# Optimization experiments

Hardware: AMD Instinct MI355X
Metric: run time of the kernel (lower is better)

Reference implementation:

```python
import jax, jax.numpy as jnp
import numpy as np

E = 8          # n_routed_experts
TOP_K = 2      # num_experts_per_tok
H = 1024       # hidden_size
I = 512        # moe_intermediate_size
SI = 512       # shared expert intermediate (I * n_shared_experts)
B, S = 4, 4096


def setup_inputs() -> dict:
    key = jax.random.key(0)
    ks = jax.random.split(key, 8)
    sc_h = 1.0 / np.sqrt(H)
    sc_i = 1.0 / np.sqrt(I)
    return {
        "hidden_states": jax.random.normal(ks[0], (B, S, H), jnp.float32),
        "gate_w": jax.random.normal(ks[1], (E, H), jnp.float32) * sc_h,  # router logits weight [E,H]
        "Wg": jax.random.normal(ks[2], (E, H, I), jnp.float32) * sc_h,   # per-expert gate_proj
        "Wu": jax.random.normal(ks[3], (E, H, I), jnp.float32) * sc_h,   # per-expert up_proj
        "Wd": jax.random.normal(ks[4], (E, I, H), jnp.float32) * sc_i,   # per-expert down_proj
        "sWg": jax.random.normal(ks[5], (H, SI), jnp.float32) * sc_h,    # shared expert gate_proj
        "sWu": jax.random.normal(ks[6], (H, SI), jnp.float32) * sc_h,
        "sWd": jax.random.normal(ks[7], (SI, H), jnp.float32) * sc_i,
    }


def reference(hidden_states, gate_w, Wg, Wu, Wd, sWg, sWu, sWd):
    b, s, h = hidden_states.shape
    x = hidden_states.reshape(-1, h)                      # [T,H]

    # ---- MoEGate: softmax scoring + greedy top-k + weight normalization ----
    logits = x.astype(jnp.float32) @ gate_w.T             # [T,E]
    scores = jax.nn.softmax(logits, axis=-1)
    topk_w, topk_idx = jax.lax.top_k(scores, TOP_K)       # [T,K]
    topk_w = topk_w / (topk_w.sum(-1, keepdims=True) + 1e-20)  # norm_topk_prob

    # combine weights as a dense [T,E] map (scatter of topk weights)
    cw = (jax.nn.one_hot(topk_idx, E, dtype=topk_w.dtype) * topk_w[..., None]).sum(1)  # [T,E]

    # ---- routed experts: down(gelu(gate(x)) * up(x)), combined by gate weight ----
    g = jnp.einsum("th,ehi->tei", x, Wg)
    u = jnp.einsum("th,ehi->tei", x, Wu)
    inter = jax.nn.gelu(g, approximate=False) * u         # [T,E,I]
    y = jnp.einsum("tei,te,eih->th", inter, cw.astype(x.dtype), Wd)

    # ---- shared expert on the identity path ----
    sh = (jax.nn.gelu(x @ sWg, approximate=False) * (x @ sWu)) @ sWd

    return (y + sh).reshape(b, s, h)
```

## Files before the change

kernel.cpp:

```cpp
#include <hip/hip_runtime.h>
#include <hip/hip_bf16.h>
#include <math.h>


#define T_TOTAL 16384
#define HDIM 1024
#define IDIM 512
#define NE 9
#define CNT_STRIDE 16

typedef __bf16 bf16x8 __attribute__((ext_vector_type(8)));
typedef float f32x4 __attribute__((ext_vector_type(4)));

typedef __attribute__((address_space(1))) void gvoid_t;
typedef __attribute__((address_space(3))) void lvoid_t;

__device__ __forceinline__ void load_lds16(const void* g, void* l) {
  __builtin_amdgcn_global_load_lds((const gvoid_t*)g, (lvoid_t*)l, 16, 0, 0);
}

__device__ __forceinline__ f32x4 mfma_bf16(bf16x8 a, bf16x8 b, f32x4 c) {
  return __builtin_amdgcn_mfma_f32_16x16x32_bf16(a, b, c, 0, 0, 0);
}

__global__ __launch_bounds__(256) void k_gate(const float* __restrict__ x,
                                              const float* __restrict__ gw,
                                              __bf16* __restrict__ xb,
                                              int* __restrict__ tok,
                                              float* __restrict__ wtl,
                                              int* __restrict__ cnt,
                                              int* __restrict__ inv) {
  __shared__ int s_eid[64][2];
  __shared__ float s_wt[64][2];
  __shared__ int s_rank[64][2];
  __shared__ int lcnt[8];
  __shared__ int lbase[8];
  const int wv = threadIdx.x >> 6, lane = threadIdx.x & 63;
  if (threadIdx.x < 8) lcnt[threadIdx.x] = 0;
  __syncthreads();

  for (int i = 0; i < 16; i++) {
    const int tl = wv * 16 + i;
    const int t = blockIdx.x * 64 + tl;
    const float* xr = x + (size_t)t * HDIM + lane * 16;
    float4 xv[4];
#pragma unroll
    for (int j = 0; j < 4; j++) xv[j] = ((const float4*)xr)[j];

    bf16x8 v0, v1;
#pragma unroll
    for (int j = 0; j < 8; j++) v0[j] = (__bf16)((const float*)xv)[j];
#pragma unroll
    for (int j = 0; j < 8; j++) v1[j] = (__bf16)((const float*)xv)[j + 8];
    bf16x8* xbo = (bf16x8*)(xb + (size_t)t * HDIM + lane * 16);
    xbo[0] = v0;
    xbo[1] = v1;

    float acc[8];
#pragma unroll
    for (int e = 0; e < 8; e++) {
      const float4* gp = (const float4*)(gw + e * HDIM + lane * 16);
      float s = 0.f;
#pragma unroll
      for (int j = 0; j < 4; j++) {
        float4 g = gp[j];
        s += xv[j].x * g.x + xv[j].y * g.y + xv[j].z * g.z + xv[j].w * g.w;
      }
      acc[e] = s;
    }
#pragma unroll
    for (int d = 32; d >= 1; d >>= 1) {
#pragma unroll
      for (int e = 0; e < 8; e++) acc[e] += __shfl_xor(acc[e], d, 64);
    }
    if (lane == 0) {
      float mx = acc[0];
#pragma unroll
      for (int e = 1; e < 8; e++) mx = fmaxf(mx, acc[e]);
      float p[8], Z = 0.f;
#pragma unroll
      for (int e = 0; e < 8; e++) {
        p[e] = expf(acc[e] - mx);
        Z += p[e];
      }
#pragma unroll
      for (int e = 0; e < 8; e++) p[e] /= Z;
      int i1 = 0;
#pragma unroll
      for (int e = 1; e < 8; e++)
        if (p[e] > p[i1]) i1 = e;
      int i2 = (i1 == 0) ? 1 : 0;
#pragma unroll
      for (int e = 0; e < 8; e++)
        if (e != i1 && p[e] > p[i2]) i2 = e;
      const float s12 = p[i1] + p[i2] + 1e-20f;
      s_eid[tl][0] = i1;
      s_eid[tl][1] = i2;
      s_wt[tl][0] = p[i1] / s12;
      s_wt[tl][1] = p[i2] / s12;
    }
  }
  __syncthreads();

  if (threadIdx.x < 64) {
    s_rank[threadIdx.x][0] = atomicAdd(&lcnt[s_eid[threadIdx.x][0]], 1);
    s_rank[threadIdx.x][1] = atomicAdd(&lcnt[s_eid[threadIdx.x][1]], 1);
  }
  __syncthreads();
  if (threadIdx.x < 8)
    lbase[threadIdx.x] =
        atomicAdd(&cnt[threadIdx.x * CNT_STRIDE], lcnt[threadIdx.x]);
  __syncthreads();
  if (threadIdx.x < 64) {
    const int t = blockIdx.x * 64 + threadIdx.x;
#pragma unroll
    for (int j = 0; j < 2; j++) {
      const int e = s_eid[threadIdx.x][j];
      const int slot = lbase[e] + s_rank[threadIdx.x][j];
      tok[e * T_TOTAL + slot] = t;
      wtl[e * T_TOTAL + slot] = s_wt[threadIdx.x][j];
      inv[t * 2 + j] = e * T_TOTAL + slot;
    }
  }
}

__global__ void k_scan(const int* __restrict__ cnt, int* __restrict__ base) {
  if (threadIdx.x == 0 && blockIdx.x == 0) {
    int s = 0;
#pragma unroll
    for (int e = 0; e < 8; e++) {
      base[e] = s;
      s += cnt[e * CNT_STRIDE];
    }
  }
}

__global__ __launch_bounds__(256) void k_transpose64(
    const float* __restrict__ w8, const float* __restrict__ w1,
    __bf16* __restrict__ out) {
  __shared__ float tile[64][65];
  const int b = blockIdx.z;
  const float* src = (b < 8) ? (w8 + (size_t)b * IDIM * HDIM) : w1;
  const int c0 = blockIdx.x * 64, r0 = blockIdx.y * 64;
  const int t = threadIdx.x;

#pragma unroll
  for (int j = 0; j < 4; j++) {
    const int rr = (t >> 4) + j * 16;
    const int cc = (t & 15) * 4;
    const float4 v = *(const float4*)(src + (size_t)(r0 + rr) * HDIM + c0 + cc);
    tile[rr][cc] = v.x;
    tile[rr][cc + 1] = v.y;
    tile[rr][cc + 2] = v.z;
    tile[rr][cc + 3] = v.w;
  }
  __syncthreads();

#pragma unroll
  for (int j = 0; j < 2; j++) {
    const int cidx = (t >> 3) + j * 32;
    const int rseg = (t & 7) * 8;
    bf16x8 v;
#pragma unroll
    for (int k = 0; k < 8; k++) v[k] = (__bf16)tile[rseg + k][cidx];
    *(bf16x8*)(out + (size_t)b * HDIM * IDIM + (size_t)(c0 + cidx) * IDIM + r0 +
               rseg) = v;
  }
}

__global__ __launch_bounds__(256) void k_transpose_fuse64(
    const float* __restrict__ w8, const float* __restrict__ w1,
    __bf16* __restrict__ out, int u16off) {
  __shared__ float tile[64][65];
  const int b = blockIdx.z;
  const float* src = (b < 8) ? (w8 + (size_t)b * HDIM * IDIM) : w1;
  const int c0 = blockIdx.x * 64, r0 = blockIdx.y * 64;
  const int t = threadIdx.x;

#pragma unroll
  for (int j = 0; j < 4; j++) {
    const int rr = (t >> 4) + j * 16;
    const int cc = (t & 15) * 4;
    const float4 v = *(const float4*)(src + (size_t)(r0 + rr) * IDIM + c0 + cc);
    tile[rr][cc] = v.x;
    tile[rr][cc + 1] = v.y;
    tile[rr][cc + 2] = v.z;
    tile[rr][cc + 3] = v.w;
  }
  __syncthreads();

#pragma unroll
  for (int j = 0; j < 2; j++) {
    const int cidx = (t >> 3) + j * 32;
    const int rseg = (t & 7) * 8;
    const int ic = c0 + cidx;
    const int f = 2 * (ic & ~15) + (ic & 15) + u16off;
    bf16x8 v;
#pragma unroll
    for (int k = 0; k < 8; k++) v[k] = (__bf16)tile[rseg + k][cidx];
    *(bf16x8*)(out + (size_t)b * 1024 * HDIM + (size_t)f * HDIM + r0 + rseg) = v;
  }
}

__global__ __launch_bounds__(256, 2) void k_gu(
    const __bf16* __restrict__ xb, const __bf16* __restrict__ Wfu,
    const int* __restrict__ tok, const float* __restrict__ wtl,
    const int* __restrict__ cnt, __bf16* __restrict__ inter, int zbase) {
  const int e = blockIdx.z + zbase;
  const bool se = (e == 8);
  const int cnt_e = se ? T_TOTAL : cnt[e * CNT_STRIDE];
  const int m0 = blockIdx.x * 128;
  if (m0 >= cnt_e) return;

  __shared__ __bf16 sA[128][64];
  __shared__ __bf16 sB[128][64];
  const int tid = threadIdx.x, w = tid >> 6, lane = tid & 63;
  const int n0 = blockIdx.y * 128;
  const int quad = lane >> 4, l16 = lane & 15;
  const int wm = (w & 1) * 64, wn = (w >> 1) * 64;

  const int sr = tid >> 3;
  const int scs = ((tid & 7) ^ (sr & 7)) * 8;
  const __bf16* ap[4];
  const __bf16* bp[4];
#pragma unroll
  for (int sh = 0; sh < 4; sh++) {
    int s = m0 + sh * 32 + sr;
    if (s > cnt_e - 1) s = cnt_e - 1;
    const int t = se ? s : tok[e * T_TOTAL + s];
    ap[sh] = xb + (size_t)t * HDIM + scs;
    bp[sh] = Wfu + ((size_t)e * 1024 + n0 + sh * 32 + sr) * HDIM + scs;
  }
  char* const la = (char*)sA + w * 1024;
  char* const lb = (char*)sB + w * 1024;

  f32x4 acc[4][4];
#pragma unroll
  for (int im = 0; im < 4; im++)
#pragma unroll
    for (int in = 0; in < 4; in++) acc[im][in] = {0.f, 0.f, 0.f, 0.f};

  for (int k = 0; k < HDIM; k += 64) {
    __syncthreads();
#pragma unroll
    for (int sh = 0; sh < 4; sh++) {
      load_lds16(ap[sh], la + sh * 4096);
      load_lds16(bp[sh], lb + sh * 4096);
      ap[sh] += 64;
      bp[sh] += 64;
    }
    __syncthreads();
#pragma unroll
    for (int kh = 0; kh < 2; kh++) {
      bf16x8 af[4], bfr[4];
#pragma unroll
      for (int i = 0; i < 4; i++) {
        const int ra = wm + i * 16 + l16;
        af[i] = *(const bf16x8*)((const char*)sA + ra * 128 +
                                 ((kh * 4 + quad) ^ (ra & 7)) * 16);
        const int rb = wn + i * 16 + l16;
        bfr[i] = *(const bf16x8*)((const char*)sB + rb * 128 +
                                  ((kh * 4 + quad) ^ (rb & 7)) * 16);
      }
#pragma unroll
      for (int im = 0; im < 4; im++)
#pragma unroll
        for (int in = 0; in < 4; in++)
          acc[im][in] = mfma_bf16(af[im], bfr[in], acc[im][in]);
    }
  }

#pragma unroll
  for (int im = 0; im < 4; im++) {
#pragma unroll
    for (int r = 0; r < 4; r++) {
      const int slot = m0 + wm + im * 16 + quad * 4 + r;
      if (slot < cnt_e) {
        const float wt = se ? 1.0f : wtl[e * T_TOTAL + slot];
        __bf16* op =
            inter + ((size_t)e * T_TOTAL + slot) * IDIM + ((n0 + wn) >> 1) + l16;
#pragma unroll
        for (int p = 0; p < 2; p++) {
          const float g = acc[im][2 * p][r];
          const float u = acc[im][2 * p + 1][r];
          const float v =
              wt * u * 0.5f * g * (1.0f + erff(g * 0.70710678118654752f));
          op[p * 16] = (__bf16)v;
        }
      }
    }
  }
}

__global__ __launch_bounds__(256, 2) void k_down_rs(
    const __bf16* __restrict__ inter, const __bf16* __restrict__ WdT,
    const int* __restrict__ cnt, const int* __restrict__ base,
    float* __restrict__ yb) {
  const int e = blockIdx.z;
  const int cnt_e = cnt[e * CNT_STRIDE];
  const int m0 = blockIdx.x * 128;
  if (m0 >= cnt_e) return;
  const int rowb = base[e];

  __shared__ __bf16 sA[128][64];
  __shared__ __bf16 sB[128][64];
  const int tid = threadIdx.x, w = tid >> 6, lane = tid & 63;
  const int n0 = blockIdx.y * 128;
  const int quad = lane >> 4, l16 = lane & 15;
  const int wm = (w & 1) * 64, wn = (w >> 1) * 64;

  const int sr = tid >> 3;
  const int scs = ((tid & 7) ^ (sr & 7)) * 8;
  const __bf16* ap[4];
  const __bf16* bp[4];
#pragma unroll
  for (int sh = 0; sh < 4; sh++) {
    int s = m0 + sh * 32 + sr;
    if (s > cnt_e - 1) s = cnt_e - 1;
    ap[sh] = inter + ((size_t)e * T_TOTAL + s) * IDIM + scs;
    bp[sh] = WdT + ((size_t)e * HDIM + n0 + sh * 32 + sr) * IDIM + scs;
  }
  char* const la = (char*)sA + w * 1024;
  char* const lb = (char*)sB + w * 1024;

  f32x4 acc[4][4];
#pragma unroll
  for (int im = 0; im < 4; im++)
#pragma unroll
    for (int in = 0; in < 4; in++) acc[im][in] = {0.f, 0.f, 0.f, 0.f};

  for (int k = 0; k < IDIM; k += 64) {
    __syncthreads();
#pragma unroll
    for (int sh = 0; sh < 4; sh++) {
      load_lds16(ap[sh], la + sh * 4096);
      load_lds16(bp[sh], lb + sh * 4096);
      ap[sh] += 64;
      bp[sh] += 64;
    }
    __syncthreads();
#pragma unroll
    for (int kh = 0; kh < 2; kh++) {
      bf16x8 af[4], bfr[4];
#pragma unroll
      for (int i = 0; i < 4; i++) {
        const int ra = wm + i * 16 + l16;
        af[i] = *(const bf16x8*)((const char*)sA + ra * 128 +
                                 ((kh * 4 + quad) ^ (ra & 7)) * 16);
        const int rb = wn + i * 16 + l16;
        bfr[i] = *(const bf16x8*)((const char*)sB + rb * 128 +
                                  ((kh * 4 + quad) ^ (rb & 7)) * 16);
      }
#pragma unroll
      for (int im = 0; im < 4; im++)
#pragma unroll
        for (int in = 0; in < 4; in++)
          acc[im][in] = mfma_bf16(af[im], bfr[in], acc[im][in]);
    }
  }

#pragma unroll
  for (int im = 0; im < 4; im++) {
#pragma unroll
    for (int r = 0; r < 4; r++) {
      const int slot = m0 + wm + im * 16 + quad * 4 + r;
      if (slot < cnt_e) {
        float* op = yb + (size_t)(rowb + slot) * HDIM + n0 + wn + l16;
#pragma unroll
        for (int in = 0; in < 4; in++) op[in * 16] = acc[im][in][r];
      }
    }
  }
}

__global__ __launch_bounds__(256, 2) void k_down_sc(
    const __bf16* __restrict__ iA, const __bf16* __restrict__ wB,
    const float* __restrict__ yb, const int* __restrict__ inv,
    const int* __restrict__ base, float* __restrict__ out) {
  __shared__ __bf16 sA[128][64];
  __shared__ __bf16 sB[128][64];
  const int tid = threadIdx.x, w = tid >> 6, lane = tid & 63;
  const int m0 = blockIdx.x * 128, n0 = blockIdx.y * 128;
  const int quad = lane >> 4, l16 = lane & 15;
  const int wm = (w & 1) * 64, wn = (w >> 1) * 64;

  const int sr = tid >> 3;
  const int scs = ((tid & 7) ^ (sr & 7)) * 8;
  const __bf16* ap[4];
  const __bf16* bp[4];
#pragma unroll
  for (int sh = 0; sh < 4; sh++) {
    ap[sh] = iA + (size_t)(m0 + sh * 32 + sr) * IDIM + scs;
    bp[sh] = wB + (size_t)(n0 + sh * 32 + sr) * IDIM + scs;
  }
  char* const la = (char*)sA + w * 1024;
  char* const lb = (char*)sB + w * 1024;

  f32x4 acc[4][4];
#pragma unroll
  for (int im = 0; im < 4; im++)
#pragma unroll
    for (int in = 0; in < 4; in++) acc[im][in] = {0.f, 0.f, 0.f, 0.f};

  for (int k = 0; k < IDIM; k += 64) {
    __syncthreads();
#pragma unroll
    for (int sh = 0; sh < 4; sh++) {
      load_lds16(ap[sh], la + sh * 4096);
      load_lds16(bp[sh], lb + sh * 4096);
      ap[sh] += 64;
      bp[sh] += 64;
    }
    __syncthreads();
#pragma unroll
    for (int kh = 0; kh < 2; kh++) {
      bf16x8 af[4], bfr[4];
#pragma unroll
      for (int i = 0; i < 4; i++) {
        const int ra = wm + i * 16 + l16;
        af[i] = *(const bf16x8*)((const char*)sA + ra * 128 +
                                 ((kh * 4 + quad) ^ (ra & 7)) * 16);
        const int rb = wn + i * 16 + l16;
        bfr[i] = *(const bf16x8*)((const char*)sB + rb * 128 +
                                  ((kh * 4 + quad) ^ (rb & 7)) * 16);
      }
#pragma unroll
      for (int im = 0; im < 4; im++)
#pragma unroll
        for (int in = 0; in < 4; in++)
          acc[im][in] = mfma_bf16(af[im], bfr[in], acc[im][in]);
    }
  }

#pragma unroll
  for (int im = 0; im < 4; im++) {
#pragma unroll
    for (int r = 0; r < 4; r++) {
      const int t = m0 + wm + im * 16 + quad * 4 + r;
      const int v1 = inv[2 * t], v2 = inv[2 * t + 1];
      const int r1 = base[v1 >> 14] + (v1 & (T_TOTAL - 1));
      const int r2 = base[v2 >> 14] + (v2 & (T_TOTAL - 1));
      const float* y1 = yb + (size_t)r1 * HDIM + n0 + wn + l16;
      const float* y2 = yb + (size_t)r2 * HDIM + n0 + wn + l16;
      float* op = out + (size_t)t * HDIM + n0 + wn + l16;
#pragma unroll
      for (int in = 0; in < 4; in++)
        op[in * 16] = acc[im][in][r] + y1[in * 16] + y2[in * 16];
    }
  }
}

__global__ __launch_bounds__(256, 2) void k_down_s(const __bf16* __restrict__ iA,
                                                   const __bf16* __restrict__ wB,
                                                   float* __restrict__ out) {
  __shared__ __bf16 sA[128][64];
  __shared__ __bf16 sB[128][64];
  const int tid = threadIdx.x, w = tid >> 6, lane = tid & 63;
  const int m0 = blockIdx.x * 128, n0 = blockIdx.y * 128;
  const int quad = lane >> 4, l16 = lane & 15;
  const int wm = (w & 1) * 64, wn = (w >> 1) * 64;

  const int sr = tid >> 3;
  const int scs = ((tid & 7) ^ (sr & 7)) * 8;
  const __bf16* ap[4];
  const __bf16* bp[4];
#pragma unroll
  for (int sh = 0; sh < 4; sh++) {
    ap[sh] = iA + (size_t)(m0 + sh * 32 + sr) * IDIM + scs;
    bp[sh] = wB + (size_t)(n0 + sh * 32 + sr) * IDIM + scs;
  }
  char* const la = (char*)sA + w * 1024;
  char* const lb = (char*)sB + w * 1024;

  f32x4 acc[4][4];
#pragma unroll
  for (int im = 0; im < 4; im++)
#pragma unroll
    for (int in = 0; in < 4; in++) acc[im][in] = {0.f, 0.f, 0.f, 0.f};

  for (int k = 0; k < IDIM; k += 64) {
    __syncthreads();
#pragma unroll
    for (int sh = 0; sh < 4; sh++) {
      load_lds16(ap[sh], la + sh * 4096);
      load_lds16(bp[sh], lb + sh * 4096);
      ap[sh] += 64;
      bp[sh] += 64;
    }
    __syncthreads();
#pragma unroll
    for (int kh = 0; kh < 2; kh++) {
      bf16x8 af[4], bfr[4];
#pragma unroll
      for (int i = 0; i < 4; i++) {
        const int ra = wm + i * 16 + l16;
        af[i] = *(const bf16x8*)((const char*)sA + ra * 128 +
                                 ((kh * 4 + quad) ^ (ra & 7)) * 16);
        const int rb = wn + i * 16 + l16;
        bfr[i] = *(const bf16x8*)((const char*)sB + rb * 128 +
                                  ((kh * 4 + quad) ^ (rb & 7)) * 16);
      }
#pragma unroll
      for (int im = 0; im < 4; im++)
#pragma unroll
        for (int in = 0; in < 4; in++)
          acc[im][in] = mfma_bf16(af[im], bfr[in], acc[im][in]);
    }
  }

#pragma unroll
  for (int im = 0; im < 4; im++) {
#pragma unroll
    for (int r = 0; r < 4; r++) {
      const int t = m0 + wm + im * 16 + quad * 4 + r;
#pragma unroll
      for (int in = 0; in < 4; in++)
        out[(size_t)t * HDIM + n0 + wn + in * 16 + l16] = acc[im][in][r];
    }
  }
}

__global__ __launch_bounds__(256, 2) void k_down_r(
    const __bf16* __restrict__ inter, const __bf16* __restrict__ WdT,
    const int* __restrict__ tok, const int* __restrict__ cnt,
    float* __restrict__ out) {
  const int e = blockIdx.z;
  const int cnt_e = cnt[e * CNT_STRIDE];
  const int m0 = blockIdx.x * 128;
  if (m0 >= cnt_e) return;

  __shared__ __bf16 sA[128][64];
  __shared__ __bf16 sB[128][64];
  const int tid = threadIdx.x, w = tid >> 6, lane = tid & 63;
  const int n0 = blockIdx.y * 128;
  const int quad = lane >> 4, l16 = lane & 15;
  const int wm = (w & 1) * 64, wn = (w >> 1) * 64;

  const int sr = tid >> 3;
  const int scs = ((tid & 7) ^ (sr & 7)) * 8;
  const __bf16* ap[4];
  const __bf16* bp[4];
#pragma unroll
  for (int sh = 0; sh < 4; sh++) {
    int s = m0 + sh * 32 + sr;
    if (s > cnt_e - 1) s = cnt_e - 1;
    ap[sh] = inter + ((size_t)e * T_TOTAL + s) * IDIM + scs;
    bp[sh] = WdT + ((size_t)e * HDIM + n0 + sh * 32 + sr) * IDIM + scs;
  }
  char* const la = (char*)sA + w * 1024;
  char* const lb = (char*)sB + w * 1024;

  f32x4 acc[4][4];
#pragma unroll
  for (int im = 0; im < 4; im++)
#pragma unroll
    for (int in = 0; in < 4; in++) acc[im][in] = {0.f, 0.f, 0.f, 0.f};

  for (int k = 0; k < IDIM; k += 64) {
    __syncthreads();
#pragma unroll
    for (int sh = 0; sh < 4; sh++) {
      load_lds16(ap[sh], la + sh * 4096);
      load_lds16(bp[sh], lb + sh * 4096);
      ap[sh] += 64;
      bp[sh] += 64;
    }
    __syncthreads();
#pragma unroll
    for (int kh = 0; kh < 2; kh++) {
      bf16x8 af[4], bfr[4];
#pragma unroll
      for (int i = 0; i < 4; i++) {
        const int ra = wm + i * 16 + l16;
        af[i] = *(const bf16x8*)((const char*)sA + ra * 128 +
                                 ((kh * 4 + quad) ^ (ra & 7)) * 16);
        const int rb = wn + i * 16 + l16;
        bfr[i] = *(const bf16x8*)((const char*)sB + rb * 128 +
                                  ((kh * 4 + quad) ^ (rb & 7)) * 16);
      }
#pragma unroll
      for (int im = 0; im < 4; im++)
#pragma unroll
        for (int in = 0; in < 4; in++)
          acc[im][in] = mfma_bf16(af[im], bfr[in], acc[im][in]);
    }
  }

#pragma unroll
  for (int im = 0; im < 4; im++) {
#pragma unroll
    for (int r = 0; r < 4; r++) {
      const int slot = m0 + wm + im * 16 + quad * 4 + r;
      if (slot < cnt_e) {
        const int t = tok[e * T_TOTAL + slot];
#pragma unroll
        for (int in = 0; in < 4; in++)
          atomicAdd(&out[(size_t)t * HDIM + n0 + wn + in * 16 + l16],
                    acc[im][in][r]);
      }
    }
  }
}

extern "C" void kernel_launch(void* const* d_in, const int* in_sizes, int n_in,
                              void* d_out, int out_size, void* d_ws,
                              size_t ws_size, hipStream_t stream) {
  const float* x = (const float*)d_in[0];
  const float* gw = (const float*)d_in[1];
  const float* Wg = (const float*)d_in[2];
  const float* Wu = (const float*)d_in[3];
  const float* Wd = (const float*)d_in[4];
  const float* sWg = (const float*)d_in[5];
  const float* sWu = (const float*)d_in[6];
  const float* sWd = (const float*)d_in[7];
  float* out = (float*)d_out;

  char* ws = (char*)d_ws;
  size_t off = 0;
  auto alloc = [&](size_t n) {
    char* p = ws + off;
    off += (n + 255) & ~(size_t)255;
    return p;
  };
  __bf16* xb = (__bf16*)alloc((size_t)T_TOTAL * HDIM * 2);
  __bf16* Wfu = (__bf16*)alloc((size_t)NE * 1024 * HDIM * 2);
  __bf16* WdT = (__bf16*)alloc((size_t)NE * HDIM * IDIM * 2);
  int* tok = (int*)alloc((size_t)8 * T_TOTAL * 4);
  float* wtl = (float*)alloc((size_t)8 * T_TOTAL * 4);
  int* cnt = (int*)alloc(8 * CNT_STRIDE * 4);
  int* inv = (int*)alloc((size_t)T_TOTAL * 2 * 4);
  int* base = (int*)alloc(16 * 4);
  __bf16* inter = (__bf16*)alloc((size_t)NE * T_TOTAL * IDIM * 2);

  const size_t yb_bytes = (size_t)2 * T_TOTAL * HDIM * 4;
  const bool store_path = (off + yb_bytes) <= ws_size;
  float* yb = store_path ? (float*)alloc(yb_bytes) : nullptr;

  hipMemsetAsync(cnt, 0, 8 * CNT_STRIDE * 4, stream);

  k_gate<<<dim3(T_TOTAL / 64), dim3(256), 0, stream>>>(x, gw, xb, tok, wtl,
                                                       cnt, inv);
  k_transpose_fuse64<<<dim3(IDIM / 64, HDIM / 64, NE), dim3(256), 0, stream>>>(
      Wg, sWg, Wfu, 0);
  k_transpose_fuse64<<<dim3(IDIM / 64, HDIM / 64, NE), dim3(256), 0, stream>>>(
      Wu, sWu, Wfu, 16);
  k_transpose64<<<dim3(HDIM / 64, IDIM / 64, NE), dim3(256), 0, stream>>>(
      Wd, sWd, WdT);
  k_scan<<<dim3(1), dim3(64), 0, stream>>>(cnt, base);

  k_gu<<<dim3(T_TOTAL / 128, 1024 / 128, 8), dim3(256), 0, stream>>>(
      xb, Wfu, tok, wtl, cnt, inter, 0);
  k_gu<<<dim3(T_TOTAL / 128, 1024 / 128, 1), dim3(256), 0, stream>>>(
      xb, Wfu, tok, wtl, cnt, inter, 8);

  if (store_path) {
    k_down_rs<<<dim3(T_TOTAL / 128, HDIM / 128, 8), dim3(256), 0, stream>>>(
        inter, WdT, cnt, base, yb);
    k_down_sc<<<dim3(T_TOTAL / 128, HDIM / 128), dim3(256), 0, stream>>>(
        inter + (size_t)8 * T_TOTAL * IDIM, WdT + (size_t)8 * HDIM * IDIM, yb,
        inv, base, out);
  } else {
    k_down_s<<<dim3(T_TOTAL / 128, HDIM / 128), dim3(256), 0, stream>>>(
        inter + (size_t)8 * T_TOTAL * IDIM, WdT + (size_t)8 * HDIM * IDIM, out);
    k_down_r<<<dim3(T_TOTAL / 128, HDIM / 128, 8), dim3(256), 0, stream>>>(
        inter, WdT, tok, cnt, out);
  }
}
```

Measured before the change: 493.6 us.

## Compact routed intermediate buffer by expert base offsets and alias yb over dead scratch

Routed-expert intermediate rows are now stored contiguously, using prefix-sum base offsets, instead of in per-expert slabs sized to the full token count. The shared-expert rows go at a fixed offset after them. The workspace is reordered so the down-proj staging buffer yb overlaps xb and Wfu, which are dead by the time the down kernels run. This shrinks the workspace footprint, improves locality, and makes the store path more likely to fit, at the cost of relying on stream ordering for the aliasing to be safe.

```diff
diff --git a/kernel.cpp b/kernel.cpp
--- a/kernel.cpp
+++ b/kernel.cpp
@@ -8,6 +8,7 @@
 #define IDIM 512
 #define NE 9
 #define CNT_STRIDE 16
+#define SH_BASE 32768
 
 typedef __bf16 bf16x8 __attribute__((ext_vector_type(8)));
 typedef float f32x4 __attribute__((ext_vector_type(4)));
@@ -205,12 +206,14 @@
 __global__ __launch_bounds__(256, 2) void k_gu(
     const __bf16* __restrict__ xb, const __bf16* __restrict__ Wfu,
     const int* __restrict__ tok, const float* __restrict__ wtl,
-    const int* __restrict__ cnt, __bf16* __restrict__ inter, int zbase) {
+    const int* __restrict__ cnt, const int* __restrict__ base,
+    __bf16* __restrict__ inter, int zbase) {
   const int e = blockIdx.z + zbase;
   const bool se = (e == 8);
   const int cnt_e = se ? T_TOTAL : cnt[e * CNT_STRIDE];
   const int m0 = blockIdx.x * 128;
   if (m0 >= cnt_e) return;
+  const int rowb = se ? SH_BASE : base[e];
 
   __shared__ __bf16 sA[128][64];
   __shared__ __bf16 sB[128][64];
@@ -277,8 +280,8 @@
       const int slot = m0 + wm + im * 16 + quad * 4 + r;
       if (slot < cnt_e) {
         const float wt = se ? 1.0f : wtl[e * T_TOTAL + slot];
-        __bf16* op =
-            inter + ((size_t)e * T_TOTAL + slot) * IDIM + ((n0 + wn) >> 1) + l16;
+        __bf16* op = inter + ((size_t)(rowb + slot)) * IDIM +
+                     ((n0 + wn) >> 1) + l16;
 #pragma unroll
         for (int p = 0; p < 2; p++) {
           const float g = acc[im][2 * p][r];
@@ -317,7 +320,7 @@
   for (int sh = 0; sh < 4; sh++) {
     int s = m0 + sh * 32 + sr;
     if (s > cnt_e - 1) s = cnt_e - 1;
-    ap[sh] = inter + ((size_t)e * T_TOTAL + s) * IDIM + scs;
+    ap[sh] = inter + (size_t)(rowb + s) * IDIM + scs;
     bp[sh] = WdT + ((size_t)e * HDIM + n0 + sh * 32 + sr) * IDIM + scs;
   }
   char* const la = (char*)sA + w * 1024;
@@ -523,11 +526,12 @@
 __global__ __launch_bounds__(256, 2) void k_down_r(
     const __bf16* __restrict__ inter, const __bf16* __restrict__ WdT,
     const int* __restrict__ tok, const int* __restrict__ cnt,
-    float* __restrict__ out) {
+    const int* __restrict__ base, float* __restrict__ out) {
   const int e = blockIdx.z;
   const int cnt_e = cnt[e * CNT_STRIDE];
   const int m0 = blockIdx.x * 128;
   if (m0 >= cnt_e) return;
+  const int rowb = base[e];
 
   __shared__ __bf16 sA[128][64];
   __shared__ __bf16 sB[128][64];
@@ -544,7 +548,7 @@
   for (int sh = 0; sh < 4; sh++) {
     int s = m0 + sh * 32 + sr;
     if (s > cnt_e - 1) s = cnt_e - 1;
-    ap[sh] = inter + ((size_t)e * T_TOTAL + s) * IDIM + scs;
+    ap[sh] = inter + (size_t)(rowb + s) * IDIM + scs;
     bp[sh] = WdT + ((size_t)e * HDIM + n0 + sh * 32 + sr) * IDIM + scs;
   }
   char* const la = (char*)sA + w * 1024;
@@ -622,19 +626,20 @@
     off += (n + 255) & ~(size_t)255;
     return p;
   };
-  __bf16* xb = (__bf16*)alloc((size_t)T_TOTAL * HDIM * 2);
-  __bf16* Wfu = (__bf16*)alloc((size_t)NE * 1024 * HDIM * 2);
   __bf16* WdT = (__bf16*)alloc((size_t)NE * HDIM * IDIM * 2);
   int* tok = (int*)alloc((size_t)8 * T_TOTAL * 4);
   float* wtl = (float*)alloc((size_t)8 * T_TOTAL * 4);
   int* cnt = (int*)alloc(8 * CNT_STRIDE * 4);
   int* inv = (int*)alloc((size_t)T_TOTAL * 2 * 4);
   int* base = (int*)alloc(16 * 4);
-  __bf16* inter = (__bf16*)alloc((size_t)NE * T_TOTAL * IDIM * 2);
+  __bf16* inter = (__bf16*)alloc((size_t)(3 * T_TOTAL) * IDIM * 2);
+  const size_t off_persist = off;
+  __bf16* xb = (__bf16*)alloc((size_t)T_TOTAL * HDIM * 2);
+  __bf16* Wfu = (__bf16*)alloc((size_t)NE * 1024 * HDIM * 2);
 
   const size_t yb_bytes = (size_t)2 * T_TOTAL * HDIM * 4;
-  const bool store_path = (off + yb_bytes) <= ws_size;
-  float* yb = store_path ? (float*)alloc(yb_bytes) : nullptr;
+  const bool store_path = (off_persist + yb_bytes) <= ws_size;
+  float* yb = (float*)(ws + off_persist);
 
   hipMemsetAsync(cnt, 0, 8 * CNT_STRIDE * 4, stream);
 
@@ -649,20 +654,20 @@
   k_scan<<<dim3(1), dim3(64), 0, stream>>>(cnt, base);
 
   k_gu<<<dim3(T_TOTAL / 128, 1024 / 128, 8), dim3(256), 0, stream>>>(
-      xb, Wfu, tok, wtl, cnt, inter, 0);
+      xb, Wfu, tok, wtl, cnt, base, inter, 0);
   k_gu<<<dim3(T_TOTAL / 128, 1024 / 128, 1), dim3(256), 0, stream>>>(
-      xb, Wfu, tok, wtl, cnt, inter, 8);
+      xb, Wfu, tok, wtl, cnt, base, inter, 8);
 
   if (store_path) {
     k_down_rs<<<dim3(T_TOTAL / 128, HDIM / 128, 8), dim3(256), 0, stream>>>(
         inter, WdT, cnt, base, yb);
     k_down_sc<<<dim3(T_TOTAL / 128, HDIM / 128), dim3(256), 0, stream>>>(
-        inter + (size_t)8 * T_TOTAL * IDIM, WdT + (size_t)8 * HDIM * IDIM, yb,
-        inv, base, out);
+        inter + (size_t)SH_BASE * IDIM, WdT + (size_t)8 * HDIM * IDIM, yb, inv,
+        base, out);
   } else {
     k_down_s<<<dim3(T_TOTAL / 128, HDIM / 128), dim3(256), 0, stream>>>(
-        inter + (size_t)8 * T_TOTAL * IDIM, WdT + (size_t)8 * HDIM * IDIM, out);
+        inter + (size_t)SH_BASE * IDIM, WdT + (size_t)8 * HDIM * IDIM, out);
     k_down_r<<<dim3(T_TOTAL / 128, HDIM / 128, 8), dim3(256), 0, stream>>>(
-        inter, WdT, tok, cnt, out);
-  }
-}
+        inter, WdT, tok, cnt, base, out);
+  }
+}
```

After: 435.5 us. 11.8% less time.
